# Kernel tuning notes

Measured on AMD Instinct MI355X. Metric: run time of the kernel, lower is better.

Reference implementation:

```python
import jax, jax.numpy as jnp
import numpy as np

N_VOX = 4_000_000
N_CLUSTS = 50_000


def setup_inputs() -> dict:
    key = jax.random.key(0)
    k1, k2 = jax.random.split(key)
    data = jax.random.normal(k1, (N_VOX, 6), dtype=jnp.float32)
    clust_ids = jax.random.randint(k2, (N_VOX,), 0, N_CLUSTS, dtype=jnp.int32)
    return {"data": data, "clust_ids": clust_ids, "n_clusts": N_CLUSTS}


def reference(data, clust_ids, n_clusts):
    # COORD_COLS = (1, 2, 3): columns [batch, x, y, z, value, shape]
    coords = data[:, 1:4].astype(jnp.float32)            # [N, 3]
    cid = clust_ids
    ones = jnp.ones((coords.shape[0],), coords.dtype)
    size = jax.ops.segment_sum(ones, cid, num_segments=n_clusts)          # [K]
    csum = jax.ops.segment_sum(coords, cid, num_segments=n_clusts)        # [K, 3]
    center = csum / jnp.maximum(size, 1.0)[:, None]                        # [K, 3]

    x = coords - center[cid]                                               # [N, 3]
    # Per-cluster scatter matrix A = x^T x (batched over clusters)
    A = jax.ops.segment_sum(x[:, :, None] * x[:, None, :], cid,
                            num_segments=n_clusts)                         # [K, 3, 3]

    w, v = jnp.linalg.eigh(A)            # ascending eigenvalues, like torch
    w2 = w[:, 2]
    safe_w2 = jnp.where(w2 > 0, w2, 1.0)
    dirwt = 1.0 - w[:, 1] / safe_w2      # [K]
    B = A / safe_w2[:, None, None]       # [K, 3, 3]
    v0 = v[:, :, 2]                      # principal axis, [K, 3]

    # Orient principal axis: sc = sum_i x0_i * ||x_i - x0_i v0||
    x0 = jnp.einsum('nd,nd->n', x, v0[cid])                                # [N]
    xp0 = x - x0[:, None] * v0[cid]                                        # [N, 3]
    np0 = jnp.linalg.norm(xp0, axis=1)                                     # [N]
    sc = jax.ops.segment_sum(x0 * np0, cid, num_segments=n_clusts)         # [K]
    v0 = jnp.where(sc[:, None] < 0, -v0, v0) * dirwt[:, None]

    # Singleton clusters (size < 2): center + 12 zeros + size
    multi = size >= 2.0
    B = jnp.where(multi[:, None, None], B, 0.0)
    v0 = jnp.where(multi[:, None], v0, 0.0)

    feats = jnp.concatenate(
        [center, B.reshape(-1, 9), v0, size[:, None]], axis=1)            # [K, 16]
    return feats
```

## Files before the change

kernel.cpp:

```cpp
#include <hip/hip_runtime.h>
#include <math.h>


#define NB_CL   64
#define CAP2    6144
#define NB_MAX  1024

__device__ inline void eig3_sym(double a00, double a01, double a02,
                                double a11, double a12, double a22,
                                double& w0, double& w1, double& w2,
                                double v[3]) {
    double p1 = a01 * a01 + a02 * a02 + a12 * a12;
    double q  = (a00 + a11 + a22) / 3.0;
    double d0 = a00 - q, d1 = a11 - q, d2 = a22 - q;
    double p2 = d0 * d0 + d1 * d1 + d2 * d2 + 2.0 * p1;
    double p  = sqrt(p2 / 6.0);
    if (p < 1e-300) {
        w0 = w1 = w2 = q;
        v[0] = 0.0; v[1] = 0.0; v[2] = 1.0;
        return;
    }
    double ip = 1.0 / p;
    double b00 = d0 * ip, b11 = d1 * ip, b22 = d2 * ip;
    double b01 = a01 * ip, b02 = a02 * ip, b12 = a12 * ip;
    double detB = b00 * (b11 * b22 - b12 * b12)
                - b01 * (b01 * b22 - b12 * b02)
                + b02 * (b01 * b12 - b11 * b02);
    double r = detB * 0.5;
    r = fmin(1.0, fmax(-1.0, r));
    double phi = acos(r) / 3.0;
    w2 = q + 2.0 * p * cos(phi);
    w0 = q + 2.0 * p * cos(phi + 2.0943951023931953);
    w1 = 3.0 * q - w2 - w0;

    double r0x = a00 - w2, r0y = a01,       r0z = a02;
    double r1x = a01,      r1y = a11 - w2,  r1z = a12;
    double r2x = a02,      r2y = a12,       r2z = a22 - w2;

    double c0x = r0y * r1z - r0z * r1y;
    double c0y = r0z * r1x - r0x * r1z;
    double c0z = r0x * r1y - r0y * r1x;
    double n0  = c0x * c0x + c0y * c0y + c0z * c0z;

    double c1x = r0y * r2z - r0z * r2y;
    double c1y = r0z * r2x - r0x * r2z;
    double c1z = r0x * r2y - r0y * r2x;
    double n1  = c1x * c1x + c1y * c1y + c1z * c1z;

    double c2x = r1y * r2z - r1z * r2y;
    double c2y = r1z * r2x - r1x * r2z;
    double c2z = r1x * r2y - r1y * r2x;
    double n2  = c2x * c2x + c2y * c2y + c2z * c2z;

    double vx, vy, vz, nn;
    if (n0 >= n1 && n0 >= n2) { vx = c0x; vy = c0y; vz = c0z; nn = n0; }
    else if (n1 >= n2)        { vx = c1x; vy = c1y; vz = c1z; nn = n1; }
    else                      { vx = c2x; vy = c2y; vz = c2z; nn = n2; }
    if (nn < 1e-300) {
        v[0] = 0.0; v[1] = 0.0; v[2] = 1.0;
        return;
    }
    double inv = rsqrt(nn);
    v[0] = vx * inv; v[1] = vy * inv; v[2] = vz * inv;
}

#define P1_BLOCK 1024
#define P1_ITEMS 8

__global__ void p1_bucket(const float* __restrict__ data,
                          const int* __restrict__ cid,
                          unsigned int* __restrict__ gcnt,
                          float4* __restrict__ bbuf,
                          int n_vox, int nbuckets) {
    __shared__ unsigned int hist[NB_MAX];
    __shared__ unsigned int base[NB_MAX];
    const int tid = threadIdx.x;
    const int per_round = P1_BLOCK * P1_ITEMS;
    const int total_rounds = (n_vox + per_round - 1) / per_round;

    for (int r = blockIdx.x; r < total_rounds; r += gridDim.x) {
        const int start = r * per_round;
        for (int j = tid; j < nbuckets; j += P1_BLOCK) hist[j] = 0;
        __syncthreads();

        int   bk[P1_ITEMS];
        int   cd[P1_ITEMS];
        float px[P1_ITEMS], py[P1_ITEMS], pz[P1_ITEMS];
        unsigned int rk[P1_ITEMS];
#pragma unroll
        for (int k = 0; k < P1_ITEMS; ++k) {
            int i = start + tid + k * P1_BLOCK;
            if (i < n_vox) {
                int c = cid[i];
                cd[k] = c & (NB_CL - 1);
                bk[k] = c >> 6;
                const float* row = data + (size_t)i * 6;
                px[k] = row[1]; py[k] = row[2]; pz[k] = row[3];
                rk[k] = atomicAdd(&hist[bk[k]], 1u);
            } else {
                bk[k] = -1;
            }
        }
        __syncthreads();
        for (int j = tid; j < nbuckets; j += P1_BLOCK) {
            unsigned int h = hist[j];
            base[j] = h ? atomicAdd(&gcnt[j], h) : 0u;
        }
        __syncthreads();
#pragma unroll
        for (int k = 0; k < P1_ITEMS; ++k) {
            if (bk[k] >= 0) {
                unsigned int pos = base[bk[k]] + rk[k];
                if (pos < (unsigned int)CAP2) {
                    bbuf[(size_t)bk[k] * CAP2 + pos] =
                        make_float4(px[k], py[k], pz[k], __int_as_float(cd[k]));
                }
            }
        }
        __syncthreads();
    }
}

__global__ __launch_bounds__(1024) void p2_features(
        const unsigned int* __restrict__ gcnt,
        const float4* __restrict__ bbuf,
        float* __restrict__ out, int C) {
    __shared__ float sx[CAP2];
    __shared__ float sy[CAP2];
    __shared__ float sz[CAP2];
    __shared__ unsigned int hist[NB_CL];
    __shared__ unsigned int basex[NB_CL];
    __shared__ unsigned int hist2[NB_CL];
    __shared__ float mom[9][NB_CL];
    __shared__ float cenl[3][NB_CL], vvl[3][NB_CL], dwl[NB_CL];

    const int b   = blockIdx.x;
    const int tid = threadIdx.x;
    const int bcnt = min((int)gcnt[b], CAP2);
    const float4* src = bbuf + (size_t)b * CAP2;

    if (tid < NB_CL) { hist[tid] = 0; hist2[tid] = 0; }
    __syncthreads();

    for (int i = tid; i < bcnt; i += 1024) {
        float4 p = src[i];
        atomicAdd(&hist[__float_as_int(p.w) & (NB_CL - 1)], 1u);
    }
    __syncthreads();

    if (tid < NB_CL) {
        unsigned int h = hist[tid];
        unsigned int inc = h;
#pragma unroll
        for (int off = 1; off < NB_CL; off <<= 1) {
            unsigned int t = __shfl_up(inc, off);
            if (tid >= off) inc += t;
        }
        basex[tid] = inc - h;
    }
    __syncthreads();

    for (int i = tid; i < bcnt; i += 1024) {
        float4 p = src[i];
        int c = __float_as_int(p.w) & (NB_CL - 1);
        unsigned int rk = atomicAdd(&hist2[c], 1u);
        unsigned int pos = basex[c] + rk;
        sx[pos] = p.x; sy[pos] = p.y; sz[pos] = p.z;
    }
    __syncthreads();

    const int w    = tid >> 6;
    const int lane = tid & 63;

#pragma unroll 1
    for (int jj = 0; jj < 4; ++jj) {
        const int lc = (w << 2) | jj;
        const int n  = (int)hist[lc];
        const unsigned int nb = basex[lc];
        float s0 = 0.f, s1 = 0.f, s2 = 0.f, s3 = 0.f, s4 = 0.f;
        float s5 = 0.f, s6 = 0.f, s7 = 0.f, s8 = 0.f;
        for (int j = lane; j < n; j += 64) {
            float x = sx[nb + j], y = sy[nb + j], z = sz[nb + j];
            s0 += x;     s1 += y;     s2 += z;
            s3 += x * x; s4 += x * y; s5 += x * z;
            s6 += y * y; s7 += y * z; s8 += z * z;
        }
#pragma unroll
        for (int d = 32; d > 0; d >>= 1) {
            s0 += __shfl_xor(s0, d); s1 += __shfl_xor(s1, d); s2 += __shfl_xor(s2, d);
            s3 += __shfl_xor(s3, d); s4 += __shfl_xor(s4, d); s5 += __shfl_xor(s5, d);
            s6 += __shfl_xor(s6, d); s7 += __shfl_xor(s7, d); s8 += __shfl_xor(s8, d);
        }
        if (lane == 0) {
            mom[0][lc] = s0; mom[1][lc] = s1; mom[2][lc] = s2;
            mom[3][lc] = s3; mom[4][lc] = s4; mom[5][lc] = s5;
            mom[6][lc] = s6; mom[7][lc] = s7; mom[8][lc] = s8;
        }
    }
    __syncthreads();

    if (tid < NB_CL) {
        const int t  = tid;
        const int cl = b * NB_CL + t;
        if (cl < C) {
            const int n = (int)hist[t];
            double dn = (double)n;
            double nd = (double)max(n, 1);
            double cx = (double)mom[0][t] / nd;
            double cy = (double)mom[1][t] / nd;
            double cz = (double)mom[2][t] / nd;

            double axx = (double)mom[3][t] - dn * cx * cx;
            double axy = (double)mom[4][t] - dn * cx * cy;
            double axz = (double)mom[5][t] - dn * cx * cz;
            double ayy = (double)mom[6][t] - dn * cy * cy;
            double ayz = (double)mom[7][t] - dn * cy * cz;
            double azz = (double)mom[8][t] - dn * cz * cz;

            double w0, w1, w2, v[3];
            eig3_sym(axx, axy, axz, ayy, ayz, azz, w0, w1, w2, v);

            double safe_w2 = (w2 > 0.0) ? w2 : 1.0;
            double isw = 1.0 / safe_w2;
            bool multi = (n >= 2);

            float fcx = (float)cx, fcy = (float)cy, fcz = (float)cz;
            float b3  = multi ? (float)(axx * isw) : 0.0f;
            float b4  = multi ? (float)(axy * isw) : 0.0f;
            float b5  = multi ? (float)(axz * isw) : 0.0f;
            float b7  = multi ? (float)(ayy * isw) : 0.0f;
            float b8  = multi ? (float)(ayz * isw) : 0.0f;
            float b11 = multi ? (float)(azz * isw) : 0.0f;

            float4* o = (float4*)(out + (size_t)cl * 16);
            o[0] = make_float4(fcx, fcy, fcz, b3);
            o[1] = make_float4(b4, b5, b4, b7);
            o[2] = make_float4(b8, b5, b8, b11);

            cenl[0][t] = fcx; cenl[1][t] = fcy; cenl[2][t] = fcz;
            vvl[0][t] = (float)v[0]; vvl[1][t] = (float)v[1]; vvl[2][t] = (float)v[2];
            dwl[t] = (float)(1.0 - w1 / safe_w2);
        }
    }
    __syncthreads();

#pragma unroll 1
    for (int jj = 0; jj < 4; ++jj) {
        const int lc = (w << 2) | jj;
        const int cl = b * NB_CL + lc;
        if (cl >= C) continue;
        const int n = (int)hist[lc];
        const unsigned int nb = basex[lc];
        const float fcx = cenl[0][lc], fcy = cenl[1][lc], fcz = cenl[2][lc];
        const float vx = vvl[0][lc], vy = vvl[1][lc], vz = vvl[2][lc];
        float sc = 0.0f;
        for (int j = lane; j < n; j += 64) {
            float x = sx[nb + j] - fcx, y = sy[nb + j] - fcy, z = sz[nb + j] - fcz;
            float x0 = x * vx + y * vy + z * vz;
            float qx = x - x0 * vx, qy = y - x0 * vy, qz = z - x0 * vz;
            sc += x0 * sqrtf(qx * qx + qy * qy + qz * qz);
        }
#pragma unroll
        for (int d = 32; d > 0; d >>= 1) sc += __shfl_xor(sc, d);

        if (lane == 0) {
            float sgn = (sc < 0.0f) ? -1.0f : 1.0f;
            float m = (n >= 2) ? sgn * dwl[lc] : 0.0f;
            ((float4*)(out + (size_t)cl * 16))[3] =
                make_float4(vx * m, vy * m, vz * m, (float)n);
        }
    }
}

#define FXP_SCALE 131072.0f
#define FXP_BIAS  4194304
#define FXP_INV   (1.0 / 131072.0)

__device__ __forceinline__ unsigned int fxp_enc(float v) {
    return (unsigned int)(__float2int_rn(v * FXP_SCALE) + FXP_BIAS);
}
__device__ __forceinline__ double fxp_dec(unsigned int s, int n) {
    return (double)((long long)s - (long long)n * FXP_BIAS) * FXP_INV;
}

__global__ void k1_accum(const float* __restrict__ data,
                         const int* __restrict__ cid,
                         unsigned long long* __restrict__ acc,
                         int n_vox) {
    int stride = gridDim.x * blockDim.x;
    for (int i = blockIdx.x * blockDim.x + threadIdx.x; i < n_vox; i += stride) {
        int c = cid[i];
        const float* row = data + (size_t)i * 6;
        float x = row[1], y = row[2], z = row[3];
        unsigned long long* a = acc + (size_t)c * 5;
        unsigned long long p0 = ((unsigned long long)fxp_enc(y)     << 32) | fxp_enc(x);
        unsigned long long p1 = ((unsigned long long)fxp_enc(x * x) << 32) | fxp_enc(z);
        unsigned long long p2 = ((unsigned long long)fxp_enc(x * z) << 32) | fxp_enc(x * y);
        unsigned long long p3 = ((unsigned long long)fxp_enc(y * z) << 32) | fxp_enc(y * y);
        unsigned long long p4 = (1ULL << 32)                               | fxp_enc(z * z);
        atomicAdd(&a[0], p0);
        atomicAdd(&a[1], p1);
        atomicAdd(&a[2], p2);
        atomicAdd(&a[3], p3);
        atomicAdd(&a[4], p4);
    }
}

__global__ void k2_cluster(const unsigned long long* __restrict__ acc,
                           float* __restrict__ wf,
                           float* __restrict__ out, int C) {
    int c = blockIdx.x * blockDim.x + threadIdx.x;
    if (c >= C) return;
    const unsigned long long* a = acc + (size_t)c * 5;
    unsigned long long s0 = a[0], s1 = a[1], s2 = a[2], s3 = a[3], s4 = a[4];
    int n = (int)(s4 >> 32);

    double sx  = fxp_dec((unsigned int)s0,         n);
    double sy  = fxp_dec((unsigned int)(s0 >> 32), n);
    double sz  = fxp_dec((unsigned int)s1,         n);
    double sxx = fxp_dec((unsigned int)(s1 >> 32), n);
    double sxy = fxp_dec((unsigned int)s2,         n);
    double sxz = fxp_dec((unsigned int)(s2 >> 32), n);
    double syy = fxp_dec((unsigned int)s3,         n);
    double syz = fxp_dec((unsigned int)(s3 >> 32), n);
    double szz = fxp_dec((unsigned int)s4,         n);

    double nd = (double)max(n, 1);
    double cx = sx / nd, cy = sy / nd, cz = sz / nd;
    double dn = (double)n;
    double axx = sxx - dn * cx * cx;
    double axy = sxy - dn * cx * cy;
    double axz = sxz - dn * cx * cz;
    double ayy = syy - dn * cy * cy;
    double ayz = syz - dn * cy * cz;
    double azz = szz - dn * cz * cz;

    double w0, w1, w2, v[3];
    eig3_sym(axx, axy, axz, ayy, ayz, azz, w0, w1, w2, v);

    double safe_w2 = (w2 > 0.0) ? w2 : 1.0;
    double dirwt   = 1.0 - w1 / safe_w2;
    double isw     = 1.0 / safe_w2;
    bool multi = (n >= 2);

    float* o = out + (size_t)c * 16;
    o[0] = (float)cx; o[1] = (float)cy; o[2] = (float)cz;
    if (multi) {
        o[3]  = (float)(axx * isw); o[4]  = (float)(axy * isw); o[5]  = (float)(axz * isw);
        o[6]  = (float)(axy * isw); o[7]  = (float)(ayy * isw); o[8]  = (float)(ayz * isw);
        o[9]  = (float)(axz * isw); o[10] = (float)(ayz * isw); o[11] = (float)(azz * isw);
    } else {
        o[3] = 0.f; o[4] = 0.f; o[5] = 0.f; o[6] = 0.f; o[7] = 0.f;
        o[8] = 0.f; o[9] = 0.f; o[10] = 0.f; o[11] = 0.f;
    }
    o[15] = (float)n;

    wf[(size_t)C * 1 + c] = (float)cx;
    wf[(size_t)C * 2 + c] = (float)cy;
    wf[(size_t)C * 3 + c] = (float)cz;
    wf[(size_t)C * 4 + c] = (float)v[0];
    wf[(size_t)C * 5 + c] = (float)v[1];
    wf[(size_t)C * 6 + c] = (float)v[2];
    wf[(size_t)C * 7 + c] = (float)dirwt;
}

__global__ void k3_sc(const float* __restrict__ data,
                      const int* __restrict__ cid,
                      float* __restrict__ wf,
                      int n_vox, int C) {
    const float* cenx = wf + (size_t)C * 1;
    const float* ceny = wf + (size_t)C * 2;
    const float* cenz = wf + (size_t)C * 3;
    const float* v0x  = wf + (size_t)C * 4;
    const float* v0y  = wf + (size_t)C * 5;
    const float* v0z  = wf + (size_t)C * 6;
    float* sc = wf;
    int stride = gridDim.x * blockDim.x;
    for (int i = blockIdx.x * blockDim.x + threadIdx.x; i < n_vox; i += stride) {
        int c = cid[i];
        const float* row = data + (size_t)i * 6;
        float x = row[1] - cenx[c];
        float y = row[2] - ceny[c];
        float z = row[3] - cenz[c];
        float vx = v0x[c], vy = v0y[c], vz = v0z[c];
        float x0 = x * vx + y * vy + z * vz;
        float px = x - x0 * vx;
        float py = y - x0 * vy;
        float pz = z - x0 * vz;
        atomicAdd(&sc[c], x0 * sqrtf(px * px + py * py + pz * pz));
    }
}

__global__ void k4_final(const unsigned long long* __restrict__ acc,
                         const float* __restrict__ wf,
                         float* __restrict__ out, int C) {
    int c = blockIdx.x * blockDim.x + threadIdx.x;
    if (c >= C) return;
    int n = (int)(acc[(size_t)c * 5 + 4] >> 32);
    float scv = wf[c];
    float vx  = wf[(size_t)C * 4 + c];
    float vy  = wf[(size_t)C * 5 + c];
    float vz  = wf[(size_t)C * 6 + c];
    float dir = wf[(size_t)C * 7 + c];
    float sgn = (scv < 0.0f) ? -1.0f : 1.0f;
    float m = (n >= 2) ? sgn * dir : 0.0f;
    float* o = out + (size_t)c * 16;
    o[12] = vx * m;
    o[13] = vy * m;
    o[14] = vz * m;
}

extern "C" void kernel_launch(void* const* d_in, const int* in_sizes, int n_in,
                              void* d_out, int out_size, void* d_ws, size_t ws_size,
                              hipStream_t stream) {
    const float* data = (const float*)d_in[0];
    const int*   cid  = (const int*)d_in[1];
    float* out = (float*)d_out;

    int n_vox = in_sizes[1];
    int C     = out_size / 16;

    int nbuckets = (C + NB_CL - 1) / NB_CL;
    long long expected = (C > 0) ? (long long)n_vox * NB_CL / C : 0;
    size_t gcnt_bytes = ((size_t)nbuckets * 4 + 255) & ~(size_t)255;
    size_t bbuf_bytes = (size_t)nbuckets * CAP2 * 16;
    size_t need = gcnt_bytes + bbuf_bytes;

    if (C > 0 && nbuckets <= NB_MAX && expected <= (CAP2 * 7) / 8 && ws_size >= need) {
        unsigned int* gcnt = (unsigned int*)d_ws;
        float4* bbuf = (float4*)((char*)d_ws + gcnt_bytes);
        hipMemsetAsync(d_ws, 0, gcnt_bytes, stream);
        int total_rounds = (n_vox + P1_BLOCK * P1_ITEMS - 1) / (P1_BLOCK * P1_ITEMS);
        int p1_blocks = total_rounds < 1024 ? total_rounds : 1024;
        if (p1_blocks < 1) p1_blocks = 1;
        p1_bucket<<<p1_blocks, P1_BLOCK, 0, stream>>>(data, cid, gcnt, bbuf, n_vox, nbuckets);
        p2_features<<<nbuckets, 1024, 0, stream>>>(gcnt, bbuf, out, C);
    } else {
        unsigned long long* acc = (unsigned long long*)d_ws;
        float* wf = (float*)((char*)d_ws + (size_t)C * 40);
        hipMemsetAsync(d_ws, 0, (size_t)C * 44, stream);
        const int vox_blocks = 4096;
        const int cl_blocks  = (C + 255) / 256;
        k1_accum<<<vox_blocks, 256, 0, stream>>>(data, cid, acc, n_vox);
        k2_cluster<<<cl_blocks, 256, 0, stream>>>(acc, wf, out, C);
        k3_sc<<<vox_blocks, 256, 0, stream>>>(data, cid, wf, n_vox, C);
        k4_final<<<cl_blocks, 256, 0, stream>>>(acc, wf, out, C);
    }
}
```

Measured before the change: 147.9 us.

## Halve p2 block size, keep per-cluster stats in registers, batch bucket loads

p2_features now runs with 512 threads instead of 1024, so each wavefront owns 8 clusters instead of 4. Per-cluster moments, centers, axes and dirwt now stay in registers and are passed around with lane shuffles. This drops the shared-memory arrays and two block-wide barriers, and lets each wave do its own eigen solve. The histogram and scatter loops now issue four independent loads per thread before the atomics, to add memory-level parallelism. The trade-off is fewer threads per block, more registers per thread, and 8 lanes per wave running the double-precision eigen solve.

```diff
diff --git a/kernel.cpp b/kernel.cpp
--- a/kernel.cpp
+++ b/kernel.cpp
@@ -121,7 +121,7 @@
     }
 }
 
-__global__ __launch_bounds__(1024) void p2_features(
+__global__ __launch_bounds__(512) void p2_features(
         const unsigned int* __restrict__ gcnt,
         const float4* __restrict__ bbuf,
         float* __restrict__ out, int C) {
@@ -131,20 +131,27 @@
     __shared__ unsigned int hist[NB_CL];
     __shared__ unsigned int basex[NB_CL];
     __shared__ unsigned int hist2[NB_CL];
-    __shared__ float mom[9][NB_CL];
-    __shared__ float cenl[3][NB_CL], vvl[3][NB_CL], dwl[NB_CL];
 
     const int b   = blockIdx.x;
     const int tid = threadIdx.x;
     const int bcnt = min((int)gcnt[b], CAP2);
     const float4* src = bbuf + (size_t)b * CAP2;
+    const float*  srcw = (const float*)src;
 
     if (tid < NB_CL) { hist[tid] = 0; hist2[tid] = 0; }
     __syncthreads();
 
-    for (int i = tid; i < bcnt; i += 1024) {
-        float4 p = src[i];
-        atomicAdd(&hist[__float_as_int(p.w) & (NB_CL - 1)], 1u);
+    for (int base_i = 0; base_i < bcnt; base_i += 2048) {
+        int i0 = base_i + tid, i1 = i0 + 512, i2 = i0 + 1024, i3 = i0 + 1536;
+        int c0 = -1, c1 = -1, c2 = -1, c3 = -1;
+        if (i0 < bcnt) c0 = __float_as_int(srcw[4 * i0 + 3]) & (NB_CL - 1);
+        if (i1 < bcnt) c1 = __float_as_int(srcw[4 * i1 + 3]) & (NB_CL - 1);
+        if (i2 < bcnt) c2 = __float_as_int(srcw[4 * i2 + 3]) & (NB_CL - 1);
+        if (i3 < bcnt) c3 = __float_as_int(srcw[4 * i3 + 3]) & (NB_CL - 1);
+        if (c0 >= 0) atomicAdd(&hist[c0], 1u);
+        if (c1 >= 0) atomicAdd(&hist[c1], 1u);
+        if (c2 >= 0) atomicAdd(&hist[c2], 1u);
+        if (c3 >= 0) atomicAdd(&hist[c3], 1u);
     }
     __syncthreads();
 
@@ -160,21 +167,30 @@
     }
     __syncthreads();
 
-    for (int i = tid; i < bcnt; i += 1024) {
-        float4 p = src[i];
-        int c = __float_as_int(p.w) & (NB_CL - 1);
-        unsigned int rk = atomicAdd(&hist2[c], 1u);
-        unsigned int pos = basex[c] + rk;
-        sx[pos] = p.x; sy[pos] = p.y; sz[pos] = p.z;
+    for (int base_i = 0; base_i < bcnt; base_i += 2048) {
+        int i0 = base_i + tid, i1 = i0 + 512, i2 = i0 + 1024, i3 = i0 + 1536;
+        bool v0 = i0 < bcnt, v1 = i1 < bcnt, v2 = i2 < bcnt, v3 = i3 < bcnt;
+        float4 p0, p1, p2, p3;
+        if (v0) p0 = src[i0];
+        if (v1) p1 = src[i1];
+        if (v2) p2 = src[i2];
+        if (v3) p3 = src[i3];
+        if (v0) { int c = __float_as_int(p0.w) & (NB_CL - 1); unsigned r = atomicAdd(&hist2[c], 1u); unsigned q = basex[c] + r; sx[q] = p0.x; sy[q] = p0.y; sz[q] = p0.z; }
+        if (v1) { int c = __float_as_int(p1.w) & (NB_CL - 1); unsigned r = atomicAdd(&hist2[c], 1u); unsigned q = basex[c] + r; sx[q] = p1.x; sy[q] = p1.y; sz[q] = p1.z; }
+        if (v2) { int c = __float_as_int(p2.w) & (NB_CL - 1); unsigned r = atomicAdd(&hist2[c], 1u); unsigned q = basex[c] + r; sx[q] = p2.x; sy[q] = p2.y; sz[q] = p2.z; }
+        if (v3) { int c = __float_as_int(p3.w) & (NB_CL - 1); unsigned r = atomicAdd(&hist2[c], 1u); unsigned q = basex[c] + r; sx[q] = p3.x; sy[q] = p3.y; sz[q] = p3.z; }
     }
     __syncthreads();
 
     const int w    = tid >> 6;
     const int lane = tid & 63;
 
-#pragma unroll 1
-    for (int jj = 0; jj < 4; ++jj) {
-        const int lc = (w << 2) | jj;
+    float k0 = 0.f, k1 = 0.f, k2 = 0.f, k3 = 0.f, k4 = 0.f;
+    float k5 = 0.f, k6 = 0.f, k7 = 0.f, k8 = 0.f;
+
+#pragma unroll
+    for (int jj = 0; jj < 8; ++jj) {
+        const int lc = (w << 3) | jj;
         const int n  = (int)hist[lc];
         const unsigned int nb = basex[lc];
         float s0 = 0.f, s1 = 0.f, s2 = 0.f, s3 = 0.f, s4 = 0.f;
@@ -191,68 +207,66 @@
             s3 += __shfl_xor(s3, d); s4 += __shfl_xor(s4, d); s5 += __shfl_xor(s5, d);
             s6 += __shfl_xor(s6, d); s7 += __shfl_xor(s7, d); s8 += __shfl_xor(s8, d);
         }
-        if (lane == 0) {
-            mom[0][lc] = s0; mom[1][lc] = s1; mom[2][lc] = s2;
-            mom[3][lc] = s3; mom[4][lc] = s4; mom[5][lc] = s5;
-            mom[6][lc] = s6; mom[7][lc] = s7; mom[8][lc] = s8;
-        }
-    }
-    __syncthreads();
-
-    if (tid < NB_CL) {
-        const int t  = tid;
-        const int cl = b * NB_CL + t;
+        if (lane == jj) {
+            k0 = s0; k1 = s1; k2 = s2; k3 = s3; k4 = s4;
+            k5 = s5; k6 = s6; k7 = s7; k8 = s8;
+        }
+    }
+
+    float cenx = 0.f, ceny = 0.f, cenz = 0.f;
+    float evx = 0.f, evy = 0.f, evz = 0.f, fdw = 0.f;
+    if (lane < 8) {
+        const int lc = (w << 3) | lane;
+        const int cl = b * NB_CL + lc;
+        const int n  = (int)hist[lc];
+        double dn = (double)n;
+        double nd = (double)max(n, 1);
+        double cx = (double)k0 / nd;
+        double cy = (double)k1 / nd;
+        double cz = (double)k2 / nd;
+
+        double axx = (double)k3 - dn * cx * cx;
+        double axy = (double)k4 - dn * cx * cy;
+        double axz = (double)k5 - dn * cx * cz;
+        double ayy = (double)k6 - dn * cy * cy;
+        double ayz = (double)k7 - dn * cy * cz;
+        double azz = (double)k8 - dn * cz * cz;
+
+        double w0, w1, w2, v[3];
+        eig3_sym(axx, axy, axz, ayy, ayz, azz, w0, w1, w2, v);
+
+        double safe_w2 = (w2 > 0.0) ? w2 : 1.0;
+        double isw = 1.0 / safe_w2;
+        bool multi = (n >= 2);
+
+        cenx = (float)cx; ceny = (float)cy; cenz = (float)cz;
+        evx = (float)v[0]; evy = (float)v[1]; evz = (float)v[2];
+        fdw = (float)(1.0 - w1 / safe_w2);
+
         if (cl < C) {
-            const int n = (int)hist[t];
-            double dn = (double)n;
-            double nd = (double)max(n, 1);
-            double cx = (double)mom[0][t] / nd;
-            double cy = (double)mom[1][t] / nd;
-            double cz = (double)mom[2][t] / nd;
-
-            double axx = (double)mom[3][t] - dn * cx * cx;
-            double axy = (double)mom[4][t] - dn * cx * cy;
-            double axz = (double)mom[5][t] - dn * cx * cz;
-            double ayy = (double)mom[6][t] - dn * cy * cy;
-            double ayz = (double)mom[7][t] - dn * cy * cz;
-            double azz = (double)mom[8][t] - dn * cz * cz;
-
-            double w0, w1, w2, v[3];
-            eig3_sym(axx, axy, axz, ayy, ayz, azz, w0, w1, w2, v);
-
-            double safe_w2 = (w2 > 0.0) ? w2 : 1.0;
-            double isw = 1.0 / safe_w2;
-            bool multi = (n >= 2);
-
-            float fcx = (float)cx, fcy = (float)cy, fcz = (float)cz;
             float b3  = multi ? (float)(axx * isw) : 0.0f;
             float b4  = multi ? (float)(axy * isw) : 0.0f;
             float b5  = multi ? (float)(axz * isw) : 0.0f;
             float b7  = multi ? (float)(ayy * isw) : 0.0f;
             float b8  = multi ? (float)(ayz * isw) : 0.0f;
             float b11 = multi ? (float)(azz * isw) : 0.0f;
-
             float4* o = (float4*)(out + (size_t)cl * 16);
-            o[0] = make_float4(fcx, fcy, fcz, b3);
+            o[0] = make_float4(cenx, ceny, cenz, b3);
             o[1] = make_float4(b4, b5, b4, b7);
             o[2] = make_float4(b8, b5, b8, b11);
-
-            cenl[0][t] = fcx; cenl[1][t] = fcy; cenl[2][t] = fcz;
-            vvl[0][t] = (float)v[0]; vvl[1][t] = (float)v[1]; vvl[2][t] = (float)v[2];
-            dwl[t] = (float)(1.0 - w1 / safe_w2);
-        }
-    }
-    __syncthreads();
+        }
+    }
 
 #pragma unroll 1
-    for (int jj = 0; jj < 4; ++jj) {
-        const int lc = (w << 2) | jj;
+    for (int jj = 0; jj < 8; ++jj) {
+        const int lc = (w << 3) | jj;
         const int cl = b * NB_CL + lc;
         if (cl >= C) continue;
         const int n = (int)hist[lc];
         const unsigned int nb = basex[lc];
-        const float fcx = cenl[0][lc], fcy = cenl[1][lc], fcz = cenl[2][lc];
-        const float vx = vvl[0][lc], vy = vvl[1][lc], vz = vvl[2][lc];
+        const float fcx = __shfl(cenx, jj), fcy = __shfl(ceny, jj), fcz = __shfl(cenz, jj);
+        const float vx = __shfl(evx, jj), vy = __shfl(evy, jj), vz = __shfl(evz, jj);
+        const float dwv = __shfl(fdw, jj);
         float sc = 0.0f;
         for (int j = lane; j < n; j += 64) {
             float x = sx[nb + j] - fcx, y = sy[nb + j] - fcy, z = sz[nb + j] - fcz;
@@ -265,7 +279,7 @@
 
         if (lane == 0) {
             float sgn = (sc < 0.0f) ? -1.0f : 1.0f;
-            float m = (n >= 2) ? sgn * dwl[lc] : 0.0f;
+            float m = (n >= 2) ? sgn * dwv : 0.0f;
             ((float4*)(out + (size_t)cl * 16))[3] =
                 make_float4(vx * m, vy * m, vz * m, (float)n);
         }
@@ -434,7 +448,7 @@
         int p1_blocks = total_rounds < 1024 ? total_rounds : 1024;
         if (p1_blocks < 1) p1_blocks = 1;
         p1_bucket<<<p1_blocks, P1_BLOCK, 0, stream>>>(data, cid, gcnt, bbuf, n_vox, nbuckets);
-        p2_features<<<nbuckets, 1024, 0, stream>>>(gcnt, bbuf, out, C);
+        p2_features<<<nbuckets, 512, 0, stream>>>(gcnt, bbuf, out, C);
     } else {
         unsigned long long* acc = (unsigned long long*)d_ws;
         float* wf = (float*)((char*)d_ws + (size_t)C * 40);
```

After: 140.9 us. -4.7%, faster.
